# Kernel tuning notes

Measured on AMD Instinct MI355X. Metric: run time of the kernel, lower is better.

Reference implementation:

```python
import jax, jax.numpy as jnp
import numpy as np

B = 1024
P = 8
D = 2048
NUM_IDS = 64
MARGIN = 0.3
EPS = 1e-12


def setup_inputs() -> dict:
    key = jax.random.key(0)
    k1, k2, k3 = jax.random.split(key, 3)
    feats = jax.random.normal(k1, (B, P * D), dtype=jnp.float32)
    labels = jax.random.randint(k2, (B,), 0, NUM_IDS, dtype=jnp.int64)
    subs = jax.random.randint(k3, (B,), 0, 2, dtype=jnp.int64)
    return {"feats": feats, "labels": labels, "subs": subs}


def reference(feats, labels, subs):
    b = feats.shape[0]
    f = feats.reshape(b, -1, D)  # [B, P, D]
    dt = f.dtype

    # Per-sample class centers via a single segment-mean pass
    # (equivalent to the original per-sample boolean-mask mean loop).
    seg_sum = jax.ops.segment_sum(f, labels, num_segments=NUM_IDS)  # [NUM_IDS, P, D]
    counts = jax.ops.segment_sum(jnp.ones((b,), dt), labels, num_segments=NUM_IDS)
    centers_by_id = seg_sum / jnp.maximum(counts, 1.0)[:, None, None]
    centers = centers_by_id[labels]  # [B, P, D]

    # dist_ap[i] = sum_p ||f[i,p] - center[i,p]||
    d_ap = jnp.sqrt(jnp.clip(jnp.sum((f - centers) ** 2, axis=-1), EPS, None)).sum(-1)  # [B]
    dist_ap = d_ap[:, None] + d_ap[None, :]  # [B, B]

    # pairwise_distance: dist_aa[i,j] = sum_p ||f[i,p] - f[j,p]||, via gemm trick
    sq = jnp.sum(f * f, axis=-1)  # [B, P]
    inner = jnp.einsum('ipd,jpd->ijp', f, f)  # [B, B, P]
    d2 = sq[:, None, :] + sq[None, :, :] - 2.0 * inner
    dist_aa = jnp.sqrt(jnp.clip(d2, EPS, None)).sum(-1)  # [B, B]

    # masked margin loss over negative (different-label) pairs
    mask = labels[:, None] != labels[None, :]  # [B, B] bool
    vals = jnp.clip(dist_ap - dist_aa + MARGIN, 0.0, None)
    maskf = mask.astype(dt)
    loss = jnp.sum(vals * maskf) / jnp.sum(maskf)
    return loss
```

## Files before the change

kernel.cpp:

```cpp
#include <hip/hip_runtime.h>
#include <hip/hip_bf16.h>

#define B_ 1024
#define P_ 8
#define D_ 2048
#define FD_ (P_ * D_)
#define NID 64
#define MARGIN_ 0.3f
#define EPS_ 1e-12f

typedef unsigned short u16;
typedef float float4_t __attribute__((ext_vector_type(4)));

#define AS1 __attribute__((address_space(1)))
#define AS3 __attribute__((address_space(3)))

__device__ __forceinline__ float bf2f(u16 v) {
    unsigned x = (unsigned)v << 16;
    float f;
    __builtin_memcpy(&f, &x, 4);
    return f;
}

static const size_t OFF_COUNTS = 0;
static const size_t OFF_OFFS   = 256;
static const size_t OFF_PERM   = 512;
static const size_t OFF_NEG    = 4608;
static const size_t OFF_POS    = 8176;
static const size_t OFF_S      = 8192;
static const size_t OFF_SQ     = 40960;
static const size_t OFF_DAP    = 73728;
static const size_t OFF_FB     = 131072;
static const size_t OFF_PD     = OFF_FB + (size_t)B_ * FD_;

__global__ void k_counts(const int* __restrict__ labels, float* countsf, int* offs,
                         int* perm, float* negcnt) {
    __shared__ int h[NID], o[NID], cur[NID];
    int tid = threadIdx.x;
    if (tid < NID) h[tid] = 0;
    __syncthreads();
    for (int i = tid; i < B_; i += 256) atomicAdd(&h[labels[i]], 1);
    __syncthreads();
    if (tid == 0) {
        int acc = 0;
        long long ss = 0;
        for (int c = 0; c < NID; c++) {
            o[c] = acc;
            acc += h[c];
            ss += (long long)h[c] * h[c];
        }
        *negcnt = (float)((long long)B_ * B_ - ss);
    }
    __syncthreads();
    if (tid < NID) {
        countsf[tid] = (float)h[tid];
        offs[tid] = o[tid];
        cur[tid] = o[tid];
    }
    __syncthreads();
    for (int i = tid; i < B_; i += 256) {
        int pos = atomicAdd(&cur[labels[i]], 1);
        perm[pos] = i;
    }
}

__global__ void k_rowstats(const float* __restrict__ feats, unsigned char* __restrict__ fb,
                           float* __restrict__ sq) {
    int i = blockIdx.x;
    int tid = threadIdx.x;
    int w = tid >> 6, lane = tid & 63;
    const float* frow = feats + (size_t)i * FD_;
    unsigned char* brow = fb + (size_t)i * FD_;
#pragma unroll
    for (int pp = 0; pp < 2; pp++) {
        int p = w * 2 + pp;
        int off = p * D_;
        float s2 = 0.f;
#pragma unroll
        for (int ch = 0; ch < 8; ch++) {
            int d = off + ch * 256 + lane * 4;
            float4 f = *(const float4*)(frow + d);
            int pk = __builtin_amdgcn_cvt_pk_fp8_f32(f.x, f.y, 0, false);
            pk = __builtin_amdgcn_cvt_pk_fp8_f32(f.z, f.w, pk, true);
            *(unsigned int*)(brow + d) = (unsigned int)pk;
            s2 += f.x * f.x + f.y * f.y + f.z * f.z + f.w * f.w;
        }
        for (int o = 32; o; o >>= 1) s2 += __shfl_down(s2, o, 64);
        if (lane == 0) sq[i * P_ + p] = s2;
    }
}

__global__ __launch_bounds__(512, 4) void k_pairs(const unsigned char* __restrict__ fb,
                                                  const float* __restrict__ sq,
                                                  const int* __restrict__ labels,
                                                  float* __restrict__ S,
                                                  u16* __restrict__ pd) {
    const int i0 = blockIdx.y * 128, j0 = blockIdx.x * 128;
    const int p = blockIdx.z;
    __shared__ __align__(16) unsigned char smem[65536];
    __shared__ float sqAs[128], sqBs[128];
    __shared__ int labA[128], labB[128];
    const int tid = threadIdx.x;
    const int lane = tid & 63, wid = tid >> 6;
    const int s = wid & 3, h = wid >> 2;
    if (tid < 128) {
        sqAs[tid] = sq[(i0 + tid) * 8 + p];
        labA[tid] = labels[i0 + tid];
    } else if (tid < 256) {
        int t = tid - 128;
        sqBs[t] = sq[(j0 + t) * 8 + p];
        labB[t] = labels[j0 + t];
    }

    const int wi = (s >> 1) * 64, wj = (s & 1) * 64;
    const int lhi = lane >> 4, llo = lane & 15;
    const int sl = llo & 7;
    const int lr = lane >> 3;
    const int lc = (lane & 7) ^ lr;

    unsigned char* const As = smem + h * 16384;
    unsigned char* const Bs = smem + 32768 + h * 16384;

    const size_t colbase = (size_t)p * D_ + (size_t)h * 1024 + (size_t)lc * 16;
    const unsigned char* gA[4];
    const unsigned char* gB[4];
    unsigned char* lA[4];
    unsigned char* lB[4];
#pragma unroll
    for (int inst = 0; inst < 4; inst++) {
        int r0 = s * 32 + inst * 8;
        gA[inst] = fb + (size_t)(i0 + r0 + lr) * FD_ + colbase;
        gB[inst] = fb + (size_t)(j0 + r0 + lr) * FD_ + colbase;
        lA[inst] = As + r0 * 128;
        lB[inst] = Bs + r0 * 128;
    }

    float4_t acc[4][4];
#pragma unroll
    for (int a = 0; a < 4; a++)
#pragma unroll
        for (int b = 0; b < 4; b++) acc[a][b] = (float4_t){0.f, 0.f, 0.f, 0.f};

    for (int kb = 0; kb < 8; kb++) {
        const int koff = kb * 128;
        __syncthreads();
#pragma unroll
        for (int inst = 0; inst < 4; inst++) {
            __builtin_amdgcn_global_load_lds((const AS1 void*)(gA[inst] + koff),
                                             (AS3 void*)lA[inst], 16, 0, 0);
            __builtin_amdgcn_global_load_lds((const AS1 void*)(gB[inst] + koff),
                                             (AS3 void*)lB[inst], 16, 0, 0);
        }
        __syncthreads();
#pragma unroll
        for (int ks = 0; ks < 4; ks++) {
            const int pcb = ((2 * ks + (lhi >> 1)) ^ sl) * 16 + (lhi & 1) * 8;
            long af[4], bf[4];
#pragma unroll
            for (int a = 0; a < 4; a++) {
                af[a] = *(const long*)(As + (wi + a * 16 + llo) * 128 + pcb);
                bf[a] = *(const long*)(Bs + (wj + a * 16 + llo) * 128 + pcb);
            }
#pragma unroll
            for (int a = 0; a < 4; a++)
#pragma unroll
                for (int b = 0; b < 4; b++)
                    acc[a][b] = __builtin_amdgcn_mfma_f32_16x16x32_fp8_fp8(
                        af[a], bf[b], acc[a][b], 0, 0, 0);
        }
    }
    __syncthreads();
    float* ep = (float*)smem;
    if (h == 1) {
#pragma unroll
        for (int a = 0; a < 4; a++)
#pragma unroll
            for (int b = 0; b < 4; b++)
                *(float4_t*)&ep[(((s * 4 + a) * 4 + b) * 64 + lane) * 4] = acc[a][b];
    }
    __syncthreads();
    if (h == 0) {
        u16* outp = pd + (size_t)p * B_ * B_;
        float rs[4][4];
#pragma unroll
        for (int a = 0; a < 4; a++)
#pragma unroll
            for (int r = 0; r < 4; r++) rs[a][r] = 0.f;
#pragma unroll
        for (int a = 0; a < 4; a++) {
            int la0 = labA[wi + a * 16 + lhi * 4 + 0];
            int la1 = labA[wi + a * 16 + lhi * 4 + 1];
            int la2 = labA[wi + a * 16 + lhi * 4 + 2];
            int la3 = labA[wi + a * 16 + lhi * 4 + 3];
#pragma unroll
            for (int b = 0; b < 4; b++) {
                float4_t o = *(const float4_t*)&ep[(((s * 4 + a) * 4 + b) * 64 + lane) * 4];
                int lb = labB[wj + b * 16 + llo];
                int jl = wj + b * 16 + llo;
#pragma unroll
                for (int r = 0; r < 4; r++) {
                    int il = wi + a * 16 + lhi * 4 + r;
                    float t = acc[a][b][r] + o[r];
                    float d2 = sqAs[il] + sqBs[jl] - 2.0f * t;
                    outp[(size_t)(i0 + il) * B_ + (j0 + jl)] =
                        __bfloat16_as_ushort(__float2bfloat16(sqrtf(fmaxf(d2, EPS_))));
                    int la = (r == 0) ? la0 : (r == 1) ? la1 : (r == 2) ? la2 : la3;
                    if (lb == la) rs[a][r] += t;
                }
            }
        }
#pragma unroll
        for (int a = 0; a < 4; a++)
#pragma unroll
            for (int r = 0; r < 4; r++) {
                float v = rs[a][r];
                v += __shfl_xor(v, 1, 64);
                v += __shfl_xor(v, 2, 64);
                v += __shfl_xor(v, 4, 64);
                v += __shfl_xor(v, 8, 64);
                if (llo == 0)
                    atomicAdd(&S[(size_t)(i0 + wi + a * 16 + lhi * 4 + r) * 8 + p], v);
            }
    }
}

__global__ void k_dap(const float* __restrict__ S, const float* __restrict__ sq,
                      const float* __restrict__ countsf, const int* __restrict__ offs,
                      const int* __restrict__ perm, float* __restrict__ dap) {
    int c = blockIdx.x;
    int tid = threadIdx.x;
    int cnt = (int)countsf[c];
    int off = offs[c];
    __shared__ float T[8];
    if (tid < 8) {
        float t = 0.f;
        for (int m = 0; m < cnt; m++) t += S[(size_t)perm[off + m] * 8 + tid];
        T[tid] = t;
    }
    __syncthreads();
    float n = fmaxf((float)cnt, 1.f);
    float inv = 1.f / n, inv2 = inv * inv;
    for (int m = tid; m < cnt; m += 64) {
        int i = perm[off + m];
        float d = 0.f;
#pragma unroll
        for (int p = 0; p < 8; p++) {
            float d2 = sq[i * 8 + p] - 2.f * inv * S[(size_t)i * 8 + p] + inv2 * T[p];
            d += sqrtf(fmaxf(d2, EPS_));
        }
        dap[i] = d;
    }
}

__global__ void k_lossred(const u16* __restrict__ pd, const float* __restrict__ dap,
                          const int* __restrict__ labels, float* possum) {
    int i = blockIdx.x;
    int tid = threadIdx.x;
    float di = dap[i];
    int li = labels[i];
    float lsum = 0.f;
    for (int j = tid; j < B_; j += 256) {
        if (labels[j] != li) {
            float daa = 0.f;
#pragma unroll
            for (int p = 0; p < P_; p++)
                daa += bf2f(pd[(size_t)p * B_ * B_ + (size_t)i * B_ + j]);
            float v = di + dap[j] - daa + MARGIN_;
            lsum += fmaxf(v, 0.f);
        }
    }
    for (int o = 32; o; o >>= 1) lsum += __shfl_down(lsum, o, 64);
    __shared__ float red[4];
    int wid = tid >> 6, lane = tid & 63;
    if (lane == 0) red[wid] = lsum;
    __syncthreads();
    if (tid == 0) atomicAdd(possum, red[0] + red[1] + red[2] + red[3]);
}

__global__ void k_finalize(const float* possum, const float* negcnt, float* out) {
    out[0] = possum[0] / negcnt[0];
}

extern "C" void kernel_launch(void* const* d_in, const int* in_sizes, int n_in,
                              void* d_out, int out_size, void* d_ws, size_t ws_size,
                              hipStream_t stream) {
    const float* feats = (const float*)d_in[0];
    const int* labels  = (const int*)d_in[1];
    float* out = (float*)d_out;

    char* w = (char*)d_ws;
    float* countsf = (float*)(w + OFF_COUNTS);
    int* offs      = (int*)(w + OFF_OFFS);
    int* perm      = (int*)(w + OFF_PERM);
    float* negcnt  = (float*)(w + OFF_NEG);
    float* possum  = (float*)(w + OFF_POS);
    float* S       = (float*)(w + OFF_S);
    float* sq      = (float*)(w + OFF_SQ);
    float* dap     = (float*)(w + OFF_DAP);
    unsigned char* fb = (unsigned char*)(w + OFF_FB);
    u16* pd        = (u16*)(w + OFF_PD);

    hipMemsetAsync(w + OFF_POS, 0, (OFF_S - OFF_POS) + (size_t)B_ * P_ * 4, stream);

    k_counts<<<1, 256, 0, stream>>>(labels, countsf, offs, perm, negcnt);
    k_rowstats<<<B_, 256, 0, stream>>>(feats, fb, sq);
    k_pairs<<<dim3(8, 8, 8), 512, 0, stream>>>(fb, sq, labels, S, pd);
    k_dap<<<NID, 64, 0, stream>>>(S, sq, countsf, offs, perm, dap);
    k_lossred<<<B_, 256, 0, stream>>>(pd, dap, labels, possum);
    k_finalize<<<1, 1, 0, stream>>>(possum, negcnt, out);
}
```

Baseline: 169.5 us.

## Store fp8 features part-major, drop split-K in pair GEMM, vectorize loss reduction

The fp8 copy of the features is now laid out part-major ([P][B][D]), so each GEMM block reads contiguous rows for one part. The pair kernel drops its two-way K split across wave halves, along with the LDS exchange of partial accumulators in the epilogue. It now runs 256 threads over a 16-step K loop, and consecutive blocks in launch order now cover different parts. The loss reduction kernel loads four bf16 distances per thread per part with one vector load. The trade-off is half as many waves per block and a longer serial K loop per wave in exchange for less epilogue synchronisation.

```diff
diff --git a/kernel.cpp b/kernel.cpp
--- a/kernel.cpp
+++ b/kernel.cpp
@@ -15,8 +15,8 @@
 #define AS1 __attribute__((address_space(1)))
 #define AS3 __attribute__((address_space(3)))
 
-__device__ __forceinline__ float bf2f(u16 v) {
-    unsigned x = (unsigned)v << 16;
+__device__ __forceinline__ float bf2f(unsigned v) {
+    unsigned x = v << 16;
     float f;
     __builtin_memcpy(&f, &x, 4);
     return f;
@@ -68,69 +68,62 @@
                            float* __restrict__ sq) {
     int i = blockIdx.x;
     int tid = threadIdx.x;
-    int w = tid >> 6, lane = tid & 63;
-    const float* frow = feats + (size_t)i * FD_;
-    unsigned char* brow = fb + (size_t)i * FD_;
-#pragma unroll
-    for (int pp = 0; pp < 2; pp++) {
-        int p = w * 2 + pp;
-        int off = p * D_;
-        float s2 = 0.f;
-#pragma unroll
-        for (int ch = 0; ch < 8; ch++) {
-            int d = off + ch * 256 + lane * 4;
-            float4 f = *(const float4*)(frow + d);
-            int pk = __builtin_amdgcn_cvt_pk_fp8_f32(f.x, f.y, 0, false);
-            pk = __builtin_amdgcn_cvt_pk_fp8_f32(f.z, f.w, pk, true);
-            *(unsigned int*)(brow + d) = (unsigned int)pk;
-            s2 += f.x * f.x + f.y * f.y + f.z * f.z + f.w * f.w;
-        }
-        for (int o = 32; o; o >>= 1) s2 += __shfl_down(s2, o, 64);
-        if (lane == 0) sq[i * P_ + p] = s2;
-    }
-}
-
-__global__ __launch_bounds__(512, 4) void k_pairs(const unsigned char* __restrict__ fb,
+    int p = tid >> 6, lane = tid & 63;
+    const float* frow = feats + (size_t)i * FD_ + p * D_;
+    unsigned char* brow = fb + (size_t)p * B_ * D_ + (size_t)i * D_;
+    float s2 = 0.f;
+#pragma unroll
+    for (int ch = 0; ch < 8; ch++) {
+        int d = ch * 256 + lane * 4;
+        float4 f = *(const float4*)(frow + d);
+        int pk = __builtin_amdgcn_cvt_pk_fp8_f32(f.x, f.y, 0, false);
+        pk = __builtin_amdgcn_cvt_pk_fp8_f32(f.z, f.w, pk, true);
+        *(unsigned int*)(brow + d) = (unsigned int)pk;
+        s2 += f.x * f.x + f.y * f.y + f.z * f.z + f.w * f.w;
+    }
+    for (int o = 32; o; o >>= 1) s2 += __shfl_down(s2, o, 64);
+    if (lane == 0) sq[i * P_ + p] = s2;
+}
+
+__global__ __launch_bounds__(256, 4) void k_pairs(const unsigned char* __restrict__ fb,
                                                   const float* __restrict__ sq,
                                                   const int* __restrict__ labels,
                                                   float* __restrict__ S,
                                                   u16* __restrict__ pd) {
-    const int i0 = blockIdx.y * 128, j0 = blockIdx.x * 128;
-    const int p = blockIdx.z;
-    __shared__ __align__(16) unsigned char smem[65536];
+    const int p  = blockIdx.x;
+    const int j0 = blockIdx.y * 128;
+    const int i0 = blockIdx.z * 128;
+    __shared__ __align__(16) unsigned char As[16384];
+    __shared__ __align__(16) unsigned char Bs[16384];
     __shared__ float sqAs[128], sqBs[128];
     __shared__ int labA[128], labB[128];
     const int tid = threadIdx.x;
     const int lane = tid & 63, wid = tid >> 6;
-    const int s = wid & 3, h = wid >> 2;
     if (tid < 128) {
         sqAs[tid] = sq[(i0 + tid) * 8 + p];
         labA[tid] = labels[i0 + tid];
-    } else if (tid < 256) {
+    } else {
         int t = tid - 128;
         sqBs[t] = sq[(j0 + t) * 8 + p];
         labB[t] = labels[j0 + t];
     }
 
-    const int wi = (s >> 1) * 64, wj = (s & 1) * 64;
+    const int wi = (wid >> 1) * 64, wj = (wid & 1) * 64;
     const int lhi = lane >> 4, llo = lane & 15;
     const int sl = llo & 7;
     const int lr = lane >> 3;
     const int lc = (lane & 7) ^ lr;
 
-    unsigned char* const As = smem + h * 16384;
-    unsigned char* const Bs = smem + 32768 + h * 16384;
-
-    const size_t colbase = (size_t)p * D_ + (size_t)h * 1024 + (size_t)lc * 16;
+    const size_t plbase = (size_t)p * ((size_t)B_ * D_);
     const unsigned char* gA[4];
     const unsigned char* gB[4];
     unsigned char* lA[4];
     unsigned char* lB[4];
 #pragma unroll
     for (int inst = 0; inst < 4; inst++) {
-        int r0 = s * 32 + inst * 8;
-        gA[inst] = fb + (size_t)(i0 + r0 + lr) * FD_ + colbase;
-        gB[inst] = fb + (size_t)(j0 + r0 + lr) * FD_ + colbase;
+        int r0 = wid * 32 + inst * 8;
+        gA[inst] = fb + plbase + (size_t)(i0 + r0 + lr) * D_ + lc * 16;
+        gB[inst] = fb + plbase + (size_t)(j0 + r0 + lr) * D_ + lc * 16;
         lA[inst] = As + r0 * 128;
         lB[inst] = Bs + r0 * 128;
     }
@@ -141,7 +134,7 @@
 #pragma unroll
         for (int b = 0; b < 4; b++) acc[a][b] = (float4_t){0.f, 0.f, 0.f, 0.f};
 
-    for (int kb = 0; kb < 8; kb++) {
+    for (int kb = 0; kb < 16; kb++) {
         const int koff = kb * 128;
         __syncthreads();
 #pragma unroll
@@ -169,59 +162,46 @@
                         af[a], bf[b], acc[a][b], 0, 0, 0);
         }
     }
-    __syncthreads();
-    float* ep = (float*)smem;
-    if (h == 1) {
-#pragma unroll
-        for (int a = 0; a < 4; a++)
-#pragma unroll
-            for (int b = 0; b < 4; b++)
-                *(float4_t*)&ep[(((s * 4 + a) * 4 + b) * 64 + lane) * 4] = acc[a][b];
-    }
-    __syncthreads();
-    if (h == 0) {
-        u16* outp = pd + (size_t)p * B_ * B_;
-        float rs[4][4];
-#pragma unroll
-        for (int a = 0; a < 4; a++)
-#pragma unroll
-            for (int r = 0; r < 4; r++) rs[a][r] = 0.f;
-#pragma unroll
-        for (int a = 0; a < 4; a++) {
-            int la0 = labA[wi + a * 16 + lhi * 4 + 0];
-            int la1 = labA[wi + a * 16 + lhi * 4 + 1];
-            int la2 = labA[wi + a * 16 + lhi * 4 + 2];
-            int la3 = labA[wi + a * 16 + lhi * 4 + 3];
-#pragma unroll
-            for (int b = 0; b < 4; b++) {
-                float4_t o = *(const float4_t*)&ep[(((s * 4 + a) * 4 + b) * 64 + lane) * 4];
-                int lb = labB[wj + b * 16 + llo];
-                int jl = wj + b * 16 + llo;
-#pragma unroll
-                for (int r = 0; r < 4; r++) {
-                    int il = wi + a * 16 + lhi * 4 + r;
-                    float t = acc[a][b][r] + o[r];
-                    float d2 = sqAs[il] + sqBs[jl] - 2.0f * t;
-                    outp[(size_t)(i0 + il) * B_ + (j0 + jl)] =
-                        __bfloat16_as_ushort(__float2bfloat16(sqrtf(fmaxf(d2, EPS_))));
-                    int la = (r == 0) ? la0 : (r == 1) ? la1 : (r == 2) ? la2 : la3;
-                    if (lb == la) rs[a][r] += t;
-                }
+    u16* outp = pd + (size_t)p * B_ * B_;
+    float rs[4][4];
+#pragma unroll
+    for (int a = 0; a < 4; a++)
+#pragma unroll
+        for (int r = 0; r < 4; r++) rs[a][r] = 0.f;
+#pragma unroll
+    for (int a = 0; a < 4; a++) {
+        int la0 = labA[wi + a * 16 + lhi * 4 + 0];
+        int la1 = labA[wi + a * 16 + lhi * 4 + 1];
+        int la2 = labA[wi + a * 16 + lhi * 4 + 2];
+        int la3 = labA[wi + a * 16 + lhi * 4 + 3];
+#pragma unroll
+        for (int b = 0; b < 4; b++) {
+            int jl = wj + b * 16 + llo;
+            int lb = labB[jl];
+#pragma unroll
+            for (int r = 0; r < 4; r++) {
+                int il = wi + a * 16 + lhi * 4 + r;
+                float t = acc[a][b][r];
+                float d2 = sqAs[il] + sqBs[jl] - 2.0f * t;
+                outp[(size_t)(i0 + il) * B_ + (j0 + jl)] =
+                    __bfloat16_as_ushort(__float2bfloat16(sqrtf(fmaxf(d2, EPS_))));
+                int la = (r == 0) ? la0 : (r == 1) ? la1 : (r == 2) ? la2 : la3;
+                if (lb == la) rs[a][r] += t;
             }
         }
-#pragma unroll
-        for (int a = 0; a < 4; a++)
-#pragma unroll
-            for (int r = 0; r < 4; r++) {
-                float v = rs[a][r];
-                v += __shfl_xor(v, 1, 64);
-                v += __shfl_xor(v, 2, 64);
-                v += __shfl_xor(v, 4, 64);
-                v += __shfl_xor(v, 8, 64);
-                if (llo == 0)
-                    atomicAdd(&S[(size_t)(i0 + wi + a * 16 + lhi * 4 + r) * 8 + p], v);
-            }
-    }
+    }
+#pragma unroll
+    for (int a = 0; a < 4; a++)
+#pragma unroll
+        for (int r = 0; r < 4; r++) {
+            float v = rs[a][r];
+            v += __shfl_xor(v, 1, 64);
+            v += __shfl_xor(v, 2, 64);
+            v += __shfl_xor(v, 4, 64);
+            v += __shfl_xor(v, 8, 64);
+            if (llo == 0)
+                atomicAdd(&S[(size_t)(i0 + wi + a * 16 + lhi * 4 + r) * 8 + p], v);
+        }
 }
 
 __global__ void k_dap(const float* __restrict__ S, const float* __restrict__ sq,
@@ -258,16 +238,22 @@
     int tid = threadIdx.x;
     float di = dap[i];
     int li = labels[i];
+    int jb = tid * 4;
+    float daa0 = 0.f, daa1 = 0.f, daa2 = 0.f, daa3 = 0.f;
+#pragma unroll
+    for (int p = 0; p < 8; p++) {
+        uint2 v = *(const uint2*)&pd[((size_t)p << 20) + (size_t)i * B_ + jb];
+        daa0 += bf2f(v.x & 0xFFFFu);
+        daa1 += bf2f(v.x >> 16);
+        daa2 += bf2f(v.y & 0xFFFFu);
+        daa3 += bf2f(v.y >> 16);
+    }
     float lsum = 0.f;
-    for (int j = tid; j < B_; j += 256) {
-        if (labels[j] != li) {
-            float daa = 0.f;
-#pragma unroll
-            for (int p = 0; p < P_; p++)
-                daa += bf2f(pd[(size_t)p * B_ * B_ + (size_t)i * B_ + j]);
-            float v = di + dap[j] - daa + MARGIN_;
-            lsum += fmaxf(v, 0.f);
-        }
+    float daas[4] = {daa0, daa1, daa2, daa3};
+#pragma unroll
+    for (int q = 0; q < 4; q++) {
+        int j = jb + q;
+        if (labels[j] != li) lsum += fmaxf(di + dap[j] - daas[q] + MARGIN_, 0.f);
     }
     for (int o = 32; o; o >>= 1) lsum += __shfl_down(lsum, o, 64);
     __shared__ float red[4];
@@ -303,8 +289,8 @@
     hipMemsetAsync(w + OFF_POS, 0, (OFF_S - OFF_POS) + (size_t)B_ * P_ * 4, stream);
 
     k_counts<<<1, 256, 0, stream>>>(labels, countsf, offs, perm, negcnt);
-    k_rowstats<<<B_, 256, 0, stream>>>(feats, fb, sq);
-    k_pairs<<<dim3(8, 8, 8), 512, 0, stream>>>(fb, sq, labels, S, pd);
+    k_rowstats<<<B_, 512, 0, stream>>>(feats, fb, sq);
+    k_pairs<<<dim3(8, 8, 8), 256, 0, stream>>>(fb, sq, labels, S, pd);
     k_dap<<<NID, 64, 0, stream>>>(S, sq, countsf, offs, perm, dap);
     k_lossred<<<B_, 256, 0, stream>>>(pd, dap, labels, possum);
     k_finalize<<<1, 1, 0, stream>>>(possum, negcnt, out);
```

Result: slower. 174.5 us (+2.9%).
